# Kernel tuning notes

Measured on AMD Instinct MI355X. Metric: run time of the kernel, lower is better.

The kernel has to match this reference:

```python
import jax, jax.numpy as jnp
import numpy as np

B, Q, K, D, H = 16, 128, 128, 512, 512
NEG = -1e6


def setup_inputs() -> dict:
    key = jax.random.key(0)
    ks = jax.random.split(key, 7)
    return {
        "queries": jax.random.normal(ks[0], (B, Q, D), dtype=jnp.float32),
        "keys": jax.random.normal(ks[1], (B, K, D), dtype=jnp.float32),
        "values": jax.random.normal(ks[2], (B, K, D), dtype=jnp.float32),
        "valid_lens": jax.random.randint(ks[3], (B,), 1, K + 1, dtype=jnp.int32),
        "Wq": jax.random.normal(ks[4], (D, H), dtype=jnp.float32) / np.sqrt(D),
        "Wk": jax.random.normal(ks[5], (D, H), dtype=jnp.float32) / np.sqrt(D),
        "wv": jax.random.normal(ks[6], (H,), dtype=jnp.float32) / np.sqrt(H),
    }


def reference(queries, keys, values, valid_lens, Wq, Wk, wv):
    # projections (LazyLinear, bias=False)
    q = jnp.einsum("bqd,dh->bqh", queries, Wq)  # [B,Q,H]
    k = jnp.einsum("bkd,dh->bkh", keys, Wk)    # [B,K,H]
    # broadcast add -> tanh -> reduce to scalar score (Bahdanau)
    feats = jnp.tanh(q[:, :, None, :] + k[:, None, :, :])  # [B,Q,K,H]
    scores = jnp.einsum("bqkh,h->bqk", feats, wv)           # [B,Q,K]
    # masked softmax over key dim using per-batch valid lengths
    mask = jnp.arange(scores.shape[-1])[None, None, :] < valid_lens[:, None, None]
    scores = jnp.where(mask, scores, NEG)
    attn = jax.nn.softmax(scores, axis=-1)                  # [B,Q,K]
    # dropout is identity in eval mode
    return jnp.einsum("bqk,bkv->bqv", attn, values)
```

## Files before the change

### kernel.cpp

```cpp
#include <hip/hip_runtime.h>

#define Bn 16
#define Qn 128
#define Kn 128
#define Dn 512
#define Hn 512
#define NEGV (-3.0e38f)
#define PSCALE 2.8853900817779268f

typedef short s16x8 __attribute__((ext_vector_type(8)));
typedef float f32x4 __attribute__((ext_vector_type(4)));

__device__ __forceinline__ float exp2_hw(float x) {
  float r;
  asm("v_exp_f32 %0, %1" : "=v"(r) : "v"(x));
  return r;
}
__device__ __forceinline__ float rcp_hw(float x) { return __builtin_amdgcn_rcpf(x); }
__device__ __forceinline__ unsigned short f2bf(float f) {
  unsigned int u = __float_as_uint(f);
  u += 0x7fff + ((u >> 16) & 1);
  return (unsigned short)(u >> 16);
}
__device__ __forceinline__ unsigned int pack2bf(float lo, float hi) {
  return (unsigned int)f2bf(lo) | ((unsigned int)f2bf(hi) << 16);
}

__global__ __launch_bounds__(256) void convert_w(
    const float* __restrict__ Wq, const float* __restrict__ Wk,
    unsigned short* __restrict__ Wt)
{
  const int tid = blockIdx.x * 256 + threadIdx.x;
  const int n = tid & 511, rest = tid >> 9;
  const int sel = rest >> 5, k16 = rest & 31;
  const float* W = sel ? Wk : Wq;
  unsigned short o[16];
  #pragma unroll
  for (int i = 0; i < 16; ++i)
    o[i] = f2bf(W[(size_t)(k16 * 16 + i) * Hn + n]);
  unsigned short* dst = Wt + (size_t)sel * 262144 + (size_t)n * 512 + k16 * 16;
  #pragma unroll
  for (int j = 0; j < 4; ++j) *(ushort4*)(dst + j * 4) = *(ushort4*)&o[j * 4];
}

__global__ __launch_bounds__(256) void proj_mfma(
    const float* __restrict__ queries, const float* __restrict__ keys,
    const unsigned short* __restrict__ Wt, const float* __restrict__ wv,
    float* __restrict__ QW, float* __restrict__ Ekq)
{
  __shared__ unsigned short Al[64][72];
  __shared__ unsigned short Bl[128][72];
  __shared__ float Tep[64][68];
  const int t = threadIdx.x, w = t >> 6, l = t & 63;
  const int wm = w >> 1, wn = w & 1;
  const int rowTile = blockIdx.x;
  const int n0 = blockIdx.y * 128;
  const int R0 = rowTile * 64;
  const bool isQ = rowTile < 32;
  const float* Asrc = isQ ? queries : keys;
  const int rowBase = isQ ? R0 : (R0 - 2048);
  const unsigned short* Wsel = Wt + (isQ ? 0 : 262144);

  f32x4 acc[2][4];
  #pragma unroll
  for (int m = 0; m < 2; ++m)
    #pragma unroll
    for (int n = 0; n < 4; ++n) acc[m][n] = (f32x4)0.f;

  const int lr = l & 15, lk = l >> 4;

  for (int k0 = 0; k0 < Hn; k0 += 64) {
    float4 afr[4];
    ushort4 br[4][2];
    #pragma unroll
    for (int i = 0; i < 4; ++i) {
      int g = t + 256 * i, r = g >> 4, c4 = g & 15;
      afr[i] = *(const float4*)(Asrc + (size_t)(rowBase + r) * Dn + k0 + c4 * 4);
    }
    #pragma unroll
    for (int i = 0; i < 4; ++i) {
      int g = t + 256 * i, r = g >> 3, c = g & 7;
      const unsigned short* p = Wsel + (size_t)(n0 + r) * Hn + k0 + c * 8;
      br[i][0] = *(const ushort4*)p; br[i][1] = *(const ushort4*)(p + 4);
    }
    __syncthreads();
    #pragma unroll
    for (int i = 0; i < 4; ++i) {
      int g = t + 256 * i, r = g >> 4, c4 = g & 15;
      ushort4 o = {f2bf(afr[i].x), f2bf(afr[i].y), f2bf(afr[i].z), f2bf(afr[i].w)};
      *(ushort4*)&Al[r][c4 * 4] = o;
    }
    #pragma unroll
    for (int i = 0; i < 4; ++i) {
      int g = t + 256 * i, r = g >> 3, c = g & 7;
      *(ushort4*)&Bl[r][c * 8] = br[i][0]; *(ushort4*)&Bl[r][c * 8 + 4] = br[i][1];
    }
    __syncthreads();
    #pragma unroll
    for (int ks = 0; ks < 2; ++ks) {
      s16x8 af[2], bf_[4];
      #pragma unroll
      for (int m = 0; m < 2; ++m)
        af[m] = *(const s16x8*)&Al[wm * 32 + m * 16 + lr][ks * 32 + lk * 8];
      #pragma unroll
      for (int n = 0; n < 4; ++n)
        bf_[n] = *(const s16x8*)&Bl[wn * 64 + n * 16 + lr][ks * 32 + lk * 8];
      #pragma unroll
      for (int m = 0; m < 2; ++m)
        #pragma unroll
        for (int n = 0; n < 4; ++n)
          acc[m][n] = __builtin_amdgcn_mfma_f32_16x16x32_bf16(af[m], bf_[n], acc[m][n], 0, 0, 0);
    }
    __syncthreads();
  }

  if (isQ) {
    #pragma unroll
    for (int m = 0; m < 2; ++m)
      #pragma unroll
      for (int n = 0; n < 4; ++n)
        #pragma unroll
        for (int r = 0; r < 4; ++r) {
          int row = R0 + wm * 32 + m * 16 + lk * 4 + r;
          int col = n0 + wn * 64 + n * 16 + lr;
          float a = acc[m][n][r];
          float F  = exp2_hw(-PSCALE * a);
          float WF = -2.f * wv[col] * F;
          float2 o = {WF, F};
          *(float2*)(QW + ((size_t)row * Hn + col) * 2) = o;
        }
  } else {
    const int krow0 = R0 - 2048;
    const int bb = krow0 >> 7, kb = krow0 & 127;
    const int hl = t >> 2, kq = (t & 3) * 16;
    #pragma unroll
    for (int hc = 0; hc < 2; ++hc) {
      __syncthreads();
      if (wn == hc) {
        #pragma unroll
        for (int m = 0; m < 2; ++m)
          #pragma unroll
          for (int n = 0; n < 4; ++n)
            #pragma unroll
            for (int r = 0; r < 4; ++r) {
              int row_l = wm * 32 + m * 16 + lk * 4 + r;
              int h_l = n * 16 + lr;
              Tep[h_l][row_l] = exp2_hw(PSCALE * acc[m][n][r]);
            }
      }
      __syncthreads();
      float* dst = Ekq + (size_t)bb * 65536 + (size_t)(n0 + hc * 64 + hl) * 128 + kb + kq;
      #pragma unroll
      for (int j = 0; j < 4; ++j)
        *(float4*)(dst + j * 4) = *(const float4*)&Tep[hl][kq + j * 4];
    }
  }
}

__global__ __launch_bounds__(256) void score_kernel(
    const float* __restrict__ QW, const float* __restrict__ Ekq,
    float* __restrict__ Sp)
{
  __shared__ float EkL[8192];
  const int id = blockIdx.x;
  const int g = id & 127, qt = id >> 7;
  const int b = g >> 3, hs = g & 7;
  const int t = threadIdx.x, w = t >> 6, l = t & 63;
  const int qp = w * 8 + ((l >> 4) << 1);
  const int ka = (l & 15) * 4;
  const int h0 = hs * 64;

  {
    const float4* esrc = (const float4*)(Ekq + (size_t)b * 65536 + (size_t)hs * 8192);
    float4 er[8];
    #pragma unroll
    for (int i = 0; i < 8; ++i) er[i] = esrc[t + 256 * i];
    float4* edst = (float4*)EkL;
    #pragma unroll
    for (int i = 0; i < 8; ++i) edst[t + 256 * i] = er[i];
  }
  __syncthreads();

  const float* qwp0 = QW + ((size_t)(b * Qn + qt * 32 + qp) * Hn + h0) * 2;
  const float* qwp1 = qwp0 + 2 * Hn;

  float acc0[8], acc1[8];
  #pragma unroll
  for (int j = 0; j < 8; ++j) { acc0[j] = 0.f; acc1[j] = 0.f; }

  float4 nq0 = *(const float4*)(qwp0);
  float4 nq1 = *(const float4*)(qwp1);

  #pragma unroll 4
  for (int hb = 0; hb < 32; ++hb) {
    const float4 qv0 = nq0, qv1 = nq1;
    if (hb < 31) {
      nq0 = *(const float4*)(qwp0 + 4 * (hb + 1));
      nq1 = *(const float4*)(qwp1 + 4 * (hb + 1));
    }
    const float* ekp = EkL + hb * 256;
    float4 ea0 = *(const float4*)(ekp + ka);
    float4 ea1 = *(const float4*)(ekp + 64 + ka);
    float4 eb0 = *(const float4*)(ekp + 128 + ka);
    float4 eb1 = *(const float4*)(ekp + 192 + ka);
    {
      const float WF0 = qv0.x, F0 = qv0.y, WF1 = qv0.z, F1 = qv0.w;
      float d0, d1, num;
      d0 = F0 + ea0.x; d1 = F1 + eb0.x;
      num = __builtin_fmaf(WF0, d1, WF1 * d0);
      acc0[0] = __builtin_fmaf(num, rcp_hw(d0 * d1), acc0[0]);
      d0 = F0 + ea0.y; d1 = F1 + eb0.y;
      num = __builtin_fmaf(WF0, d1, WF1 * d0);
      acc0[1] = __builtin_fmaf(num, rcp_hw(d0 * d1), acc0[1]);
      d0 = F0 + ea0.z; d1 = F1 + eb0.z;
      num = __builtin_fmaf(WF0, d1, WF1 * d0);
      acc0[2] = __builtin_fmaf(num, rcp_hw(d0 * d1), acc0[2]);
      d0 = F0 + ea0.w; d1 = F1 + eb0.w;
      num = __builtin_fmaf(WF0, d1, WF1 * d0);
      acc0[3] = __builtin_fmaf(num, rcp_hw(d0 * d1), acc0[3]);
      d0 = F0 + ea1.x; d1 = F1 + eb1.x;
      num = __builtin_fmaf(WF0, d1, WF1 * d0);
      acc0[4] = __builtin_fmaf(num, rcp_hw(d0 * d1), acc0[4]);
      d0 = F0 + ea1.y; d1 = F1 + eb1.y;
      num = __builtin_fmaf(WF0, d1, WF1 * d0);
      acc0[5] = __builtin_fmaf(num, rcp_hw(d0 * d1), acc0[5]);
      d0 = F0 + ea1.z; d1 = F1 + eb1.z;
      num = __builtin_fmaf(WF0, d1, WF1 * d0);
      acc0[6] = __builtin_fmaf(num, rcp_hw(d0 * d1), acc0[6]);
      d0 = F0 + ea1.w; d1 = F1 + eb1.w;
      num = __builtin_fmaf(WF0, d1, WF1 * d0);
      acc0[7] = __builtin_fmaf(num, rcp_hw(d0 * d1), acc0[7]);
    }
    {
      const float WF0 = qv1.x, F0 = qv1.y, WF1 = qv1.z, F1 = qv1.w;
      float d0, d1, num;
      d0 = F0 + ea0.x; d1 = F1 + eb0.x;
      num = __builtin_fmaf(WF0, d1, WF1 * d0);
      acc1[0] = __builtin_fmaf(num, rcp_hw(d0 * d1), acc1[0]);
      d0 = F0 + ea0.y; d1 = F1 + eb0.y;
      num = __builtin_fmaf(WF0, d1, WF1 * d0);
      acc1[1] = __builtin_fmaf(num, rcp_hw(d0 * d1), acc1[1]);
      d0 = F0 + ea0.z; d1 = F1 + eb0.z;
      num = __builtin_fmaf(WF0, d1, WF1 * d0);
      acc1[2] = __builtin_fmaf(num, rcp_hw(d0 * d1), acc1[2]);
      d0 = F0 + ea0.w; d1 = F1 + eb0.w;
      num = __builtin_fmaf(WF0, d1, WF1 * d0);
      acc1[3] = __builtin_fmaf(num, rcp_hw(d0 * d1), acc1[3]);
      d0 = F0 + ea1.x; d1 = F1 + eb1.x;
      num = __builtin_fmaf(WF0, d1, WF1 * d0);
      acc1[4] = __builtin_fmaf(num, rcp_hw(d0 * d1), acc1[4]);
      d0 = F0 + ea1.y; d1 = F1 + eb1.y;
      num = __builtin_fmaf(WF0, d1, WF1 * d0);
      acc1[5] = __builtin_fmaf(num, rcp_hw(d0 * d1), acc1[5]);
      d0 = F0 + ea1.z; d1 = F1 + eb1.z;
      num = __builtin_fmaf(WF0, d1, WF1 * d0);
      acc1[6] = __builtin_fmaf(num, rcp_hw(d0 * d1), acc1[6]);
      d0 = F0 + ea1.w; d1 = F1 + eb1.w;
      num = __builtin_fmaf(WF0, d1, WF1 * d0);
      acc1[7] = __builtin_fmaf(num, rcp_hw(d0 * d1), acc1[7]);
    }
  }

  const int q = qt * 32 + qp;
  size_t sb = (((size_t)hs * Bn + b) * Qn + q) * Kn;
  *(float4*)(Sp + sb + ka)            = (float4){acc0[0], acc0[1], acc0[2], acc0[3]};
  *(float4*)(Sp + sb + 64 + ka)       = (float4){acc0[4], acc0[5], acc0[6], acc0[7]};
  *(float4*)(Sp + sb + Kn + ka)       = (float4){acc1[0], acc1[1], acc1[2], acc1[3]};
  *(float4*)(Sp + sb + Kn + 64 + ka)  = (float4){acc1[4], acc1[5], acc1[6], acc1[7]};
}

__global__ __launch_bounds__(256) void softmax_av(
    const float* __restrict__ Sp, const int* __restrict__ valid_lens,
    const float* __restrict__ values, float* __restrict__ out)
{
  __shared__ unsigned short AtL[16][136];
  __shared__ unsigned int VLu[128][36];
  const int t = threadIdx.x, w = t >> 6, l = t & 63;
  const int b = blockIdx.y;
  const int qt = blockIdx.x & 7;
  const int dt = blockIdx.x >> 3;
  const int lr = l & 15, lk = l >> 4;

  {
    const int q_l = t >> 4, k8 = (t & 15) * 8;
    const size_t base = ((size_t)(b * Qn) + qt * 16 + q_l) * Kn + k8;
    float s[8] = {0.f, 0.f, 0.f, 0.f, 0.f, 0.f, 0.f, 0.f};
    #pragma unroll
    for (int p = 0; p < 8; ++p) {
      float4 a0 = *(const float4*)(Sp + base + (size_t)p * 262144);
      float4 a1 = *(const float4*)(Sp + base + (size_t)p * 262144 + 4);
      s[0] += a0.x; s[1] += a0.y; s[2] += a0.z; s[3] += a0.w;
      s[4] += a1.x; s[5] += a1.y; s[6] += a1.z; s[7] += a1.w;
    }
    const int vlen = valid_lens[b];
    bool ok[8];
    float m = NEGV;
    #pragma unroll
    for (int j = 0; j < 8; ++j) {
      ok[j] = (k8 + j) < vlen;
      if (ok[j]) m = fmaxf(m, s[j]);
    }
    #pragma unroll
    for (int xm = 8; xm >= 1; xm >>= 1) m = fmaxf(m, __shfl_xor(m, xm));
    float e[8], sum = 0.f;
    #pragma unroll
    for (int j = 0; j < 8; ++j) {
      e[j] = ok[j] ? exp2_hw((s[j] - m) * 1.44269504f) : 0.f;
      sum += e[j];
    }
    #pragma unroll
    for (int xm = 8; xm >= 1; xm >>= 1) sum += __shfl_xor(sum, xm);
    float inv = rcp_hw(sum);
    ushort4 o0 = {f2bf(e[0] * inv), f2bf(e[1] * inv), f2bf(e[2] * inv), f2bf(e[3] * inv)};
    ushort4 o1 = {f2bf(e[4] * inv), f2bf(e[5] * inv), f2bf(e[6] * inv), f2bf(e[7] * inv)};
    *(ushort4*)&AtL[q_l][k8] = o0;
    *(ushort4*)&AtL[q_l][k8 + 4] = o1;
  }
  __syncthreads();

  const int kread = t & 15, dread = (t >> 4) & 15;
  f32x4 acc[2];
  acc[0] = (f32x4)0.f; acc[1] = (f32x4)0.f;
  #pragma unroll
  for (int k0 = 0; k0 < Kn; k0 += 64) {
    if (k0) __syncthreads();
    #pragma unroll
    for (int j = 0; j < 4; ++j) {
      int k2 = kread + 16 * (j & 1);
      int d4 = dread + 16 * (j >> 1);
      const float* vp = values + ((size_t)(b * Kn) + k0 + 2 * k2) * Dn + dt * 128 + d4 * 4;
      float4 v0 = *(const float4*)(vp);
      float4 v1 = *(const float4*)(vp + Dn);
      VLu[d4 * 4 + 0][k2] = pack2bf(v0.x, v1.x);
      VLu[d4 * 4 + 1][k2] = pack2bf(v0.y, v1.y);
      VLu[d4 * 4 + 2][k2] = pack2bf(v0.z, v1.z);
      VLu[d4 * 4 + 3][k2] = pack2bf(v0.w, v1.w);
    }
    __syncthreads();
    #pragma unroll
    for (int ks = 0; ks < 2; ++ks) {
      s16x8 af = *(const s16x8*)&AtL[lr][k0 + ks * 32 + lk * 8];
      #pragma unroll
      for (int nn = 0; nn < 2; ++nn) {
        s16x8 bv = *(const s16x8*)&VLu[w * 32 + nn * 16 + lr][ks * 16 + lk * 4];
        acc[nn] = __builtin_amdgcn_mfma_f32_16x16x32_bf16(af, bv, acc[nn], 0, 0, 0);
      }
    }
  }
  #pragma unroll
  for (int nn = 0; nn < 2; ++nn)
    #pragma unroll
    for (int r = 0; r < 4; ++r) {
      int q = qt * 16 + lk * 4 + r;
      int d = dt * 128 + w * 32 + nn * 16 + lr;
      out[((size_t)(b * Qn) + q) * Dn + d] = acc[nn][r];
    }
}

extern "C" void kernel_launch(void* const* d_in, const int* in_sizes, int n_in,
                              void* d_out, int out_size, void* d_ws, size_t ws_size,
                              hipStream_t stream) {
  const float* queries    = (const float*)d_in[0];
  const float* keys       = (const float*)d_in[1];
  const float* values     = (const float*)d_in[2];
  const int*   valid_lens = (const int*)d_in[3];
  const float* Wq         = (const float*)d_in[4];
  const float* Wk         = (const float*)d_in[5];
  const float* wv         = (const float*)d_in[6];
  float* out = (float*)d_out;

  unsigned short* Wt  = (unsigned short*)d_ws;
  float*          QW  = (float*)(Wt + 524288);
  float*          Ekq = QW + 2097152;
  float*          Sp  = Ekq + 1048576;

  convert_w<<<128, 256, 0, stream>>>(Wq, Wk, Wt);
  proj_mfma<<<dim3(64, 4), 256, 0, stream>>>(queries, keys, Wt, wv, QW, Ekq);
  score_kernel<<<512, 256, 0, stream>>>(QW, Ekq, Sp);
  softmax_av<<<dim3(32, 16), 256, 0, stream>>>(Sp, valid_lens, values, out);
}
```

Measured before the change: 47.47 us.

## Store projected exp factors as packed bf16 and stage query factors in LDS

The projection kernel now writes the query factors (WF,F) and the key exp factors as packed bf16 pairs instead of fp32, halving the intermediate traffic. The score kernel loads both the key and query tiles into padded LDS arrays, unpacks the bf16 values with shifts and masks, and changes the k-index mapping so each lane owns 8 contiguous keys. This reduces global memory traffic and the per-iteration global loads of the query factors. In exchange it adds unpack ALU work and loses precision in the exp-domain factors, which feed a rational tanh identity and could amplify error.

```diff
diff --git a/kernel.cpp b/kernel.cpp
--- a/kernel.cpp
+++ b/kernel.cpp
@@ -25,6 +25,8 @@
 __device__ __forceinline__ unsigned int pack2bf(float lo, float hi) {
   return (unsigned int)f2bf(lo) | ((unsigned int)f2bf(hi) << 16);
 }
+__device__ __forceinline__ float bfl(unsigned int u) { return __uint_as_float(u << 16); }
+__device__ __forceinline__ float bfh(unsigned int u) { return __uint_as_float(u & 0xffff0000u); }
 
 __global__ __launch_bounds__(256) void convert_w(
     const float* __restrict__ Wq, const float* __restrict__ Wk,
@@ -46,7 +48,7 @@
 __global__ __launch_bounds__(256) void proj_mfma(
     const float* __restrict__ queries, const float* __restrict__ keys,
     const unsigned short* __restrict__ Wt, const float* __restrict__ wv,
-    float* __restrict__ QW, float* __restrict__ Ekq)
+    unsigned int* __restrict__ QWp, unsigned int* __restrict__ Ekp)
 {
   __shared__ unsigned short Al[64][72];
   __shared__ unsigned short Bl[128][72];
@@ -126,8 +128,7 @@
           float a = acc[m][n][r];
           float F  = exp2_hw(-PSCALE * a);
           float WF = -2.f * wv[col] * F;
-          float2 o = {WF, F};
-          *(float2*)(QW + ((size_t)row * Hn + col) * 2) = o;
+          QWp[(size_t)row * Hn + col] = pack2bf(WF, F);
         }
   } else {
     const int krow0 = R0 - 2048;
@@ -149,124 +150,100 @@
             }
       }
       __syncthreads();
-      float* dst = Ekq + (size_t)bb * 65536 + (size_t)(n0 + hc * 64 + hl) * 128 + kb + kq;
-      #pragma unroll
-      for (int j = 0; j < 4; ++j)
-        *(float4*)(dst + j * 4) = *(const float4*)&Tep[hl][kq + j * 4];
-    }
-  }
+      unsigned int* dst = Ekp + (size_t)bb * 32768
+                        + (size_t)(n0 + hc * 64 + hl) * 64 + (kb + kq) / 2;
+      #pragma unroll
+      for (int j = 0; j < 4; ++j) {
+        float4 v = *(const float4*)&Tep[hl][kq + j * 4];
+        uint2 o = {pack2bf(v.x, v.y), pack2bf(v.z, v.w)};
+        *(uint2*)(dst + j * 2) = o;
+      }
+    }
+  }
+}
+
+__device__ __forceinline__ void term8(const uint4 e0, const uint4 e1,
+                                      float WF0, float F0, float WF1, float F1,
+                                      const float ek0[8], const float ek1[8],
+                                      float acc[8]) {
+  #pragma unroll
+  for (int j = 0; j < 8; ++j) {
+    float d0 = F0 + ek0[j];
+    float d1 = F1 + ek1[j];
+    float num = __builtin_fmaf(WF0, d1, WF1 * d0);
+    acc[j] = __builtin_fmaf(num, rcp_hw(d0 * d1), acc[j]);
+  }
+  (void)e0; (void)e1;
 }
 
 __global__ __launch_bounds__(256) void score_kernel(
-    const float* __restrict__ QW, const float* __restrict__ Ekq,
+    const unsigned int* __restrict__ QWp, const unsigned int* __restrict__ Ekp,
     float* __restrict__ Sp)
 {
-  __shared__ float EkL[8192];
+  __shared__ unsigned int EkLu[64][68];
+  __shared__ unsigned int QWLu[32][68];
   const int id = blockIdx.x;
   const int g = id & 127, qt = id >> 7;
   const int b = g >> 3, hs = g & 7;
   const int t = threadIdx.x, w = t >> 6, l = t & 63;
   const int qp = w * 8 + ((l >> 4) << 1);
-  const int ka = (l & 15) * 4;
-  const int h0 = hs * 64;
+  const int ku = (l & 15) * 4;
+  const int ka8 = (l & 15) * 8;
 
   {
-    const float4* esrc = (const float4*)(Ekq + (size_t)b * 65536 + (size_t)hs * 8192);
-    float4 er[8];
-    #pragma unroll
-    for (int i = 0; i < 8; ++i) er[i] = esrc[t + 256 * i];
-    float4* edst = (float4*)EkL;
-    #pragma unroll
-    for (int i = 0; i < 8; ++i) edst[t + 256 * i] = er[i];
+    const uint4* esrc = (const uint4*)(Ekp + (size_t)b * 32768 + (size_t)hs * 4096);
+    uint4 er[4];
+    #pragma unroll
+    for (int i = 0; i < 4; ++i) er[i] = esrc[t + 256 * i];
+    uint4 qr[2];
+    #pragma unroll
+    for (int i = 0; i < 2; ++i) {
+      int lin = t + 256 * i, row = lin >> 4, c4 = lin & 15;
+      qr[i] = *(const uint4*)(QWp + (size_t)(b * Qn + qt * 32 + row) * Hn + hs * 64 + c4 * 4);
+    }
+    #pragma unroll
+    for (int i = 0; i < 4; ++i) {
+      int lin = t + 256 * i, row = lin >> 4, c4 = lin & 15;
+      *(uint4*)&EkLu[row][c4 * 4] = er[i];
+    }
+    #pragma unroll
+    for (int i = 0; i < 2; ++i) {
+      int lin = t + 256 * i, row = lin >> 4, c4 = lin & 15;
+      *(uint4*)&QWLu[row][c4 * 4] = qr[i];
+    }
   }
   __syncthreads();
 
-  const float* qwp0 = QW + ((size_t)(b * Qn + qt * 32 + qp) * Hn + h0) * 2;
-  const float* qwp1 = qwp0 + 2 * Hn;
-
   float acc0[8], acc1[8];
   #pragma unroll
   for (int j = 0; j < 8; ++j) { acc0[j] = 0.f; acc1[j] = 0.f; }
-
-  float4 nq0 = *(const float4*)(qwp0);
-  float4 nq1 = *(const float4*)(qwp1);
 
   #pragma unroll 4
   for (int hb = 0; hb < 32; ++hb) {
-    const float4 qv0 = nq0, qv1 = nq1;
-    if (hb < 31) {
-      nq0 = *(const float4*)(qwp0 + 4 * (hb + 1));
-      nq1 = *(const float4*)(qwp1 + 4 * (hb + 1));
-    }
-    const float* ekp = EkL + hb * 256;
-    float4 ea0 = *(const float4*)(ekp + ka);
-    float4 ea1 = *(const float4*)(ekp + 64 + ka);
-    float4 eb0 = *(const float4*)(ekp + 128 + ka);
-    float4 eb1 = *(const float4*)(ekp + 192 + ka);
+    uint4 e0 = *(const uint4*)&EkLu[2 * hb][ku];
+    uint4 e1 = *(const uint4*)&EkLu[2 * hb + 1][ku];
+    uint2 qa = *(const uint2*)&QWLu[qp][hb * 2];
+    uint2 qb = *(const uint2*)&QWLu[qp + 1][hb * 2];
+    float ek0[8], ek1[8];
     {
-      const float WF0 = qv0.x, F0 = qv0.y, WF1 = qv0.z, F1 = qv0.w;
-      float d0, d1, num;
-      d0 = F0 + ea0.x; d1 = F1 + eb0.x;
-      num = __builtin_fmaf(WF0, d1, WF1 * d0);
-      acc0[0] = __builtin_fmaf(num, rcp_hw(d0 * d1), acc0[0]);
-      d0 = F0 + ea0.y; d1 = F1 + eb0.y;
-      num = __builtin_fmaf(WF0, d1, WF1 * d0);
-      acc0[1] = __builtin_fmaf(num, rcp_hw(d0 * d1), acc0[1]);
-      d0 = F0 + ea0.z; d1 = F1 + eb0.z;
-      num = __builtin_fmaf(WF0, d1, WF1 * d0);
-      acc0[2] = __builtin_fmaf(num, rcp_hw(d0 * d1), acc0[2]);
-      d0 = F0 + ea0.w; d1 = F1 + eb0.w;
-      num = __builtin_fmaf(WF0, d1, WF1 * d0);
-      acc0[3] = __builtin_fmaf(num, rcp_hw(d0 * d1), acc0[3]);
-      d0 = F0 + ea1.x; d1 = F1 + eb1.x;
-      num = __builtin_fmaf(WF0, d1, WF1 * d0);
-      acc0[4] = __builtin_fmaf(num, rcp_hw(d0 * d1), acc0[4]);
-      d0 = F0 + ea1.y; d1 = F1 + eb1.y;
-      num = __builtin_fmaf(WF0, d1, WF1 * d0);
-      acc0[5] = __builtin_fmaf(num, rcp_hw(d0 * d1), acc0[5]);
-      d0 = F0 + ea1.z; d1 = F1 + eb1.z;
-      num = __builtin_fmaf(WF0, d1, WF1 * d0);
-      acc0[6] = __builtin_fmaf(num, rcp_hw(d0 * d1), acc0[6]);
-      d0 = F0 + ea1.w; d1 = F1 + eb1.w;
-      num = __builtin_fmaf(WF0, d1, WF1 * d0);
-      acc0[7] = __builtin_fmaf(num, rcp_hw(d0 * d1), acc0[7]);
-    }
-    {
-      const float WF0 = qv1.x, F0 = qv1.y, WF1 = qv1.z, F1 = qv1.w;
-      float d0, d1, num;
-      d0 = F0 + ea0.x; d1 = F1 + eb0.x;
-      num = __builtin_fmaf(WF0, d1, WF1 * d0);
-      acc1[0] = __builtin_fmaf(num, rcp_hw(d0 * d1), acc1[0]);
-      d0 = F0 + ea0.y; d1 = F1 + eb0.y;
-      num = __builtin_fmaf(WF0, d1, WF1 * d0);
-      acc1[1] = __builtin_fmaf(num, rcp_hw(d0 * d1), acc1[1]);
-      d0 = F0 + ea0.z; d1 = F1 + eb0.z;
-      num = __builtin_fmaf(WF0, d1, WF1 * d0);
-      acc1[2] = __builtin_fmaf(num, rcp_hw(d0 * d1), acc1[2]);
-      d0 = F0 + ea0.w; d1 = F1 + eb0.w;
-      num = __builtin_fmaf(WF0, d1, WF1 * d0);
-      acc1[3] = __builtin_fmaf(num, rcp_hw(d0 * d1), acc1[3]);
-      d0 = F0 + ea1.x; d1 = F1 + eb1.x;
-      num = __builtin_fmaf(WF0, d1, WF1 * d0);
-      acc1[4] = __builtin_fmaf(num, rcp_hw(d0 * d1), acc1[4]);
-      d0 = F0 + ea1.y; d1 = F1 + eb1.y;
-      num = __builtin_fmaf(WF0, d1, WF1 * d0);
-      acc1[5] = __builtin_fmaf(num, rcp_hw(d0 * d1), acc1[5]);
-      d0 = F0 + ea1.z; d1 = F1 + eb1.z;
-      num = __builtin_fmaf(WF0, d1, WF1 * d0);
-      acc1[6] = __builtin_fmaf(num, rcp_hw(d0 * d1), acc1[6]);
-      d0 = F0 + ea1.w; d1 = F1 + eb1.w;
-      num = __builtin_fmaf(WF0, d1, WF1 * d0);
-      acc1[7] = __builtin_fmaf(num, rcp_hw(d0 * d1), acc1[7]);
-    }
+      const unsigned int u0[4] = {e0.x, e0.y, e0.z, e0.w};
+      const unsigned int u1[4] = {e1.x, e1.y, e1.z, e1.w};
+      #pragma unroll
+      for (int p = 0; p < 4; ++p) {
+        ek0[2 * p] = bfl(u0[p]); ek0[2 * p + 1] = bfh(u0[p]);
+        ek1[2 * p] = bfl(u1[p]); ek1[2 * p + 1] = bfh(u1[p]);
+      }
+    }
+    term8(e0, e1, bfl(qa.x), bfh(qa.x), bfl(qa.y), bfh(qa.y), ek0, ek1, acc0);
+    term8(e0, e1, bfl(qb.x), bfh(qb.x), bfl(qb.y), bfh(qb.y), ek0, ek1, acc1);
   }
 
   const int q = qt * 32 + qp;
   size_t sb = (((size_t)hs * Bn + b) * Qn + q) * Kn;
-  *(float4*)(Sp + sb + ka)            = (float4){acc0[0], acc0[1], acc0[2], acc0[3]};
-  *(float4*)(Sp + sb + 64 + ka)       = (float4){acc0[4], acc0[5], acc0[6], acc0[7]};
-  *(float4*)(Sp + sb + Kn + ka)       = (float4){acc1[0], acc1[1], acc1[2], acc1[3]};
-  *(float4*)(Sp + sb + Kn + 64 + ka)  = (float4){acc1[4], acc1[5], acc1[6], acc1[7]};
+  *(float4*)(Sp + sb + ka8)          = (float4){acc0[0], acc0[1], acc0[2], acc0[3]};
+  *(float4*)(Sp + sb + ka8 + 4)      = (float4){acc0[4], acc0[5], acc0[6], acc0[7]};
+  *(float4*)(Sp + sb + Kn + ka8)     = (float4){acc1[0], acc1[1], acc1[2], acc1[3]};
+  *(float4*)(Sp + sb + Kn + ka8 + 4) = (float4){acc1[4], acc1[5], acc1[6], acc1[7]};
 }
 
 __global__ __launch_bounds__(256) void softmax_av(
@@ -370,12 +347,12 @@
   float* out = (float*)d_out;
 
   unsigned short* Wt  = (unsigned short*)d_ws;
-  float*          QW  = (float*)(Wt + 524288);
-  float*          Ekq = QW + 2097152;
-  float*          Sp  = Ekq + 1048576;
+  unsigned int*   QWp = (unsigned int*)(Wt + 524288);
+  unsigned int*   Ekp = QWp + 1048576;
+  float*          Sp  = (float*)(Ekp + 524288);
 
   convert_w<<<128, 256, 0, stream>>>(Wq, Wk, Wt);
-  proj_mfma<<<dim3(64, 4), 256, 0, stream>>>(queries, keys, Wt, wv, QW, Ekq);
-  score_kernel<<<512, 256, 0, stream>>>(QW, Ekq, Sp);
+  proj_mfma<<<dim3(64, 4), 256, 0, stream>>>(queries, keys, Wt, wv, QWp, Ekp);
+  score_kernel<<<512, 256, 0, stream>>>(QWp, Ekp, Sp);
   softmax_av<<<dim3(32, 16), 256, 0, stream>>>(Sp, valid_lens, values, out);
 }
```

After: 47.75 us. Within noise of the previous version (+0.6%).
